# Optimization experiments

Measured on AMD Instinct MI355X. Metric: run time of the kernel, lower is better.

The kernel has to match this reference:

```python
import jax, jax.numpy as jnp
import numpy as np

B, N, T = 16, 10000, 24
E = 160000
H, O = 32, 16  # hidden_channels, out_channels


def setup_inputs() -> dict:
    key = jax.random.key(0)
    ks = jax.random.split(key, 13)
    x = jax.random.normal(ks[0], (B, N, T), jnp.float32)
    edge_index = jax.random.randint(ks[1], (2, E), 0, N)
    edge_weight = jax.random.uniform(ks[2], (E,), jnp.float32)

    def init(k, shape, fan):
        return (jax.random.normal(k, shape, jnp.float32) / np.sqrt(fan)).astype(jnp.float32)

    # torch.nn.GRU params (gate order: r, z, n)
    w_ih = init(ks[3], (3 * H, 1), 1)
    w_hh = init(ks[4], (3 * H, H), H)
    b_ih = jnp.zeros((3 * H,), jnp.float32)
    b_hh = jnp.zeros((3 * H,), jnp.float32)
    # GCNConv weights (stored [in, out]) and biases
    W1 = init(ks[5], (H, H), H)
    b1 = jnp.zeros((H,), jnp.float32)
    W2 = init(ks[6], (H, O), H)
    b2 = jnp.zeros((O,), jnp.float32)
    # final Linear(out_channels, 1), stored [O, 1]
    Wfc = init(ks[7], (O, 1), O)
    bfc = jnp.zeros((1,), jnp.float32)
    return {"x": x, "edge_index": edge_index, "edge_weight": edge_weight,
            "w_ih": w_ih, "w_hh": w_hh, "b_ih": b_ih, "b_hh": b_hh,
            "W1": W1, "b1": b1, "W2": W2, "b2": b2, "Wfc": Wfc, "bfc": bfc}


def _gru_last(x_seq, w_ih, w_hh, b_ih, b_hh):
    # x_seq: [M, T, 1] -> final hidden state [M, H]
    h_dim = w_hh.shape[1]
    xt = jnp.swapaxes(x_seq, 0, 1)            # [T, M, 1]
    gx = xt @ w_ih.T + b_ih                    # precompute input gates [T, M, 3H]

    def step(h, gxt):
        gh = h @ w_hh.T + b_hh
        xr, xz, xn = jnp.split(gxt, 3, axis=-1)
        hr, hz, hn = jnp.split(gh, 3, axis=-1)
        r = jax.nn.sigmoid(xr + hr)
        z = jax.nn.sigmoid(xz + hz)
        n = jnp.tanh(xn + r * hn)
        return (1.0 - z) * n + z * h, None

    h0 = jnp.zeros((x_seq.shape[0], h_dim), x_seq.dtype)
    hT, _ = jax.lax.scan(step, h0, gx)
    return hT


def _gcn_norm(edge_index, edge_weight, n_nodes):
    # PyG gcn_norm with added self-loops (weight 1) and symmetric D^-1/2 A D^-1/2
    loop = jnp.arange(n_nodes)
    src = jnp.concatenate([edge_index[0], loop])
    tgt = jnp.concatenate([edge_index[1], loop])
    w = jnp.concatenate([edge_weight, jnp.ones((n_nodes,), edge_weight.dtype)])
    deg = jax.ops.segment_sum(w, tgt, num_segments=n_nodes)
    dinv = jnp.where(deg > 0, jax.lax.rsqrt(jnp.where(deg > 0, deg, 1.0)), 0.0)
    norm = dinv[src] * w * dinv[tgt]
    return src, tgt, norm


def _gcn_conv(h, W, b, src, tgt, norm):
    # h: [B, N, Fin] -> [B, N, Fout]; gather from src, scatter-add to tgt
    xw = h @ W                                 # [B, N, Fout]
    msg = xw[:, src, :] * norm[None, :, None]  # [B, E+N, Fout]
    out = jnp.zeros_like(xw).at[:, tgt, :].add(msg)
    return out + b


def reference(x, edge_index, edge_weight, w_ih, w_hh, b_ih, b_hh, W1, b1, W2, b2, Wfc, bfc):
    batch, n_nodes, t_len = x.shape
    # GRU temporal encoder per station (eval mode: dropout is identity)
    x_flat = x.reshape(batch * n_nodes, t_len, 1)
    h = _gru_last(x_flat, w_ih, w_hh, b_ih, b_hh).reshape(batch, n_nodes, -1)
    src, tgt, norm = _gcn_norm(edge_index, edge_weight, n_nodes)
    h = jax.nn.relu(_gcn_conv(h, W1, b1, src, tgt, norm))
    h = _gcn_conv(h, W2, b2, src, tgt, norm)
    out = (h @ Wfc + bfc)[..., 0]              # [B, N]
    return out
```

## Files before the change

### kernel.cpp

```cpp
#include <hip/hip_runtime.h>

#define TLEN 24
#define HID 32
#define NNODES 10000

typedef __attribute__((ext_vector_type(8))) short short8;
typedef __attribute__((ext_vector_type(4))) float floatx4;
typedef __attribute__((ext_vector_type(4))) int int4v;

__device__ __forceinline__ unsigned short bf16_rne(float f) {
    unsigned u = __float_as_uint(f);
    unsigned r = u + 0x7fffu + ((u >> 16) & 1u);
    return (unsigned short)(r >> 16);
}
__device__ __forceinline__ float bf16_tof(unsigned short b) {
    return __uint_as_float(((unsigned)b) << 16);
}
__device__ __forceinline__ unsigned cvt_pk_bf16(float a, float b) {
    unsigned r;
    asm("v_cvt_pk_bf16_f32 %0, %1, %2" : "=v"(r) : "v"(a), "v"(b));
    return r;
}
__device__ __forceinline__ void split_pair(float a, float b, unsigned& hi, unsigned& lo) {
    hi = cvt_pk_bf16(a, b);
    float ar = __uint_as_float(hi << 16);
    float br = __uint_as_float(hi & 0xffff0000u);
    lo = cvt_pk_bf16(a - ar, b - br);
}

#define MFMA16(a, b, c) __builtin_amdgcn_mfma_f32_16x16x32_bf16((a), (b), (c), 0, 0, 0)

__global__ __launch_bounds__(256, 3) void gru_xw1_kernel(
    const float* __restrict__ x, const float* __restrict__ w_ih,
    const float* __restrict__ w_hh, const float* __restrict__ b_ih,
    const float* __restrict__ b_hh, const float* __restrict__ W1,
    float* __restrict__ xw1, int BN)
{
    __shared__ float xs[64][25];
    const int tid = threadIdx.x;
    const int wv = tid >> 6, lane = tid & 63;
    const int u = lane >> 4;
    const int s = lane & 15;

    for (int i = tid; i < 64 * TLEN; i += 256) {
        int sl = i / TLEN, t = i - sl * TLEN;
        int gseq = blockIdx.x * 64 + sl;
        if (gseq >= BN) gseq = BN - 1;
        xs[sl][t] = x[(size_t)gseq * TLEN + t];
    }
    __syncthreads();

    const float sc_rz = 1.4426950408889634f;
    const float sc_n  = 2.8853900817779268f;

    const int arow_g = 8 * (s >> 2) + (s & 3);
    short8 wh[6], wl[6];
#pragma unroll
    for (int G = 0; G < 3; G++) {
        float sc = (G == 2) ? sc_n : sc_rz;
#pragma unroll
        for (int hf = 0; hf < 2; hf++) {
            int row = G * 32 + arow_g + 4 * hf;
            const float* wp = w_hh + row * 32 + 8 * u;
            unsigned hib[4], lob[4];
#pragma unroll
            for (int p = 0; p < 4; p++)
                split_pair(wp[2 * p] * sc, wp[2 * p + 1] * sc, hib[p], lob[p]);
            int4v hv = {(int)hib[0], (int)hib[1], (int)hib[2], (int)hib[3]};
            int4v lv = {(int)lob[0], (int)lob[1], (int)lob[2], (int)lob[3]};
            wh[G * 2 + hf] = __builtin_bit_cast(short8, hv);
            wl[G * 2 + hf] = __builtin_bit_cast(short8, lv);
        }
    }

    floatx4 CUR[2], CPR[2], CUZ[2], CPZ[2], CUN[2], CBNI[2], CBNH[2];
#pragma unroll
    for (int hf = 0; hf < 2; hf++) {
#pragma unroll
        for (int r = 0; r < 4; r++) {
            int g = 8 * u + hf * 4 + r;
            CUR[hf][r]  = w_ih[g] * sc_rz;
            CPR[hf][r]  = (b_ih[g] + b_hh[g]) * sc_rz;
            CUZ[hf][r]  = w_ih[32 + g] * sc_rz;
            CPZ[hf][r]  = (b_ih[32 + g] + b_hh[32 + g]) * sc_rz;
            CUN[hf][r]  = w_ih[64 + g] * sc_n;
            CBNI[hf][r] = b_ih[64 + g] * sc_n;
            CBNH[hf][r] = b_hh[64 + g] * sc_n;
        }
    }

    asm volatile("" : "+v"(wh[0]), "+v"(wh[1]), "+v"(wh[2]), "+v"(wh[3]),
                      "+v"(wh[4]), "+v"(wh[5]), "+v"(wl[0]), "+v"(wl[1]),
                      "+v"(wl[2]), "+v"(wl[3]), "+v"(wl[4]), "+v"(wl[5]));
    asm volatile("" : "+v"(CUR[0]), "+v"(CUR[1]), "+v"(CPR[0]), "+v"(CPR[1]),
                      "+v"(CUZ[0]), "+v"(CUZ[1]), "+v"(CPZ[0]), "+v"(CPZ[1]));
    asm volatile("" : "+v"(CUN[0]), "+v"(CUN[1]), "+v"(CBNI[0]), "+v"(CBNI[1]),
                      "+v"(CBNH[0]), "+v"(CBNH[1]));

    float h[8];
#pragma unroll
    for (int i = 0; i < 8; i++) h[i] = 0.f;
    short8 Bh = {0, 0, 0, 0, 0, 0, 0, 0}, Bl = {0, 0, 0, 0, 0, 0, 0, 0};

    const int xrow = wv * 16 + s;

#pragma unroll 1
    for (int t = 0; t < TLEN; t++) {
        float xt = xs[xrow][t];
        floatx4 Dr0, Dr1, Dz0, Dz1;
        floatx4 Dn0 = CBNH[0], Dn1 = CBNH[1];
#pragma unroll
        for (int r = 0; r < 4; r++) {
            Dr0[r] = fmaf(xt, CUR[0][r], CPR[0][r]);
            Dr1[r] = fmaf(xt, CUR[1][r], CPR[1][r]);
            Dz0[r] = fmaf(xt, CUZ[0][r], CPZ[0][r]);
            Dz1[r] = fmaf(xt, CUZ[1][r], CPZ[1][r]);
        }
        Dr0 = MFMA16(wh[0], Bh, Dr0); Dr0 = MFMA16(wh[0], Bl, Dr0); Dr0 = MFMA16(wl[0], Bh, Dr0);
        Dr1 = MFMA16(wh[1], Bh, Dr1); Dr1 = MFMA16(wh[1], Bl, Dr1); Dr1 = MFMA16(wl[1], Bh, Dr1);
        Dz0 = MFMA16(wh[2], Bh, Dz0); Dz0 = MFMA16(wh[2], Bl, Dz0); Dz0 = MFMA16(wl[2], Bh, Dz0);
        Dz1 = MFMA16(wh[3], Bh, Dz1); Dz1 = MFMA16(wh[3], Bl, Dz1); Dz1 = MFMA16(wl[3], Bh, Dz1);
        Dn0 = MFMA16(wh[4], Bh, Dn0); Dn0 = MFMA16(wh[4], Bl, Dn0); Dn0 = MFMA16(wl[4], Bh, Dn0);
        Dn1 = MFMA16(wh[5], Bh, Dn1); Dn1 = MFMA16(wh[5], Bl, Dn1); Dn1 = MFMA16(wl[5], Bh, Dn1);

#pragma unroll
        for (int i = 0; i < 8; i++) {
            float dr = (i < 4) ? Dr0[i] : Dr1[i - 4];
            float dz = (i < 4) ? Dz0[i] : Dz1[i - 4];
            float dn = (i < 4) ? Dn0[i] : Dn1[i - 4];
            float rr = __builtin_amdgcn_rcpf(1.f + __builtin_amdgcn_exp2f(-dr));
            float zz = __builtin_amdgcn_rcpf(1.f + __builtin_amdgcn_exp2f(-dz));
            float gxn = fmaf(xt, CUN[i >> 2][i & 3], CBNI[i >> 2][i & 3]);
            float pn2 = fmaf(rr, dn, gxn);
            float e2 = __builtin_amdgcn_exp2f(pn2);
            float tnh = fmaf(-2.f, __builtin_amdgcn_rcpf(e2 + 1.f), 1.f);
            h[i] = fmaf(zz, h[i] - tnh, tnh);
        }
        unsigned hb[4], lb[4];
#pragma unroll
        for (int p = 0; p < 4; p++) split_pair(h[2 * p], h[2 * p + 1], hb[p], lb[p]);
        int4v hv = {(int)hb[0], (int)hb[1], (int)hb[2], (int)hb[3]};
        int4v lv = {(int)lb[0], (int)lb[1], (int)lb[2], (int)lb[3]};
        Bh = __builtin_bit_cast(short8, hv);
        Bl = __builtin_bit_cast(short8, lv);
    }

    short8 W1h[2], W1l[2];
#pragma unroll
    for (int tile = 0; tile < 2; tile++) {
        int o = tile * 16 + s;
        short8 a, b;
#pragma unroll
        for (int j = 0; j < 8; j++) {
            float wfull = W1[(8 * u + j) * 32 + o];
            unsigned short hbb = bf16_rne(wfull);
            float lo = wfull - bf16_tof(hbb);
            a[j] = (short)hbb;
            b[j] = (short)bf16_rne(lo);
        }
        W1h[tile] = a; W1l[tile] = b;
    }
    floatx4 X0, X1;
#pragma unroll
    for (int r = 0; r < 4; r++) { X0[r] = 0.f; X1[r] = 0.f; }
    X0 = MFMA16(W1h[0], Bh, X0); X0 = MFMA16(W1h[0], Bl, X0); X0 = MFMA16(W1l[0], Bh, X0);
    X1 = MFMA16(W1h[1], Bh, X1); X1 = MFMA16(W1h[1], Bl, X1); X1 = MFMA16(W1l[1], Bh, X1);

    int seq = blockIdx.x * 64 + wv * 16 + s;
    if (seq >= BN) seq = BN - 1;
    int bq = seq / NNODES;
    int nn = seq - bq * NNODES;
    float* base = xw1 + (size_t)nn * 512 + bq * 32 + 4 * u;
    float4 v0, v1;
    v0.x = X0[0]; v0.y = X0[1]; v0.z = X0[2]; v0.w = X0[3];
    v1.x = X1[0]; v1.y = X1[1]; v1.z = X1[2]; v1.w = X1[3];
    *reinterpret_cast<float4*>(base) = v0;
    *reinterpret_cast<float4*>(base + 16) = v1;
}

__global__ void init_deg_cnt(float* deg, int* cnt, int N)
{
    int i = blockIdx.x * 256 + threadIdx.x;
    if (i < N) { deg[i] = 1.0f; cnt[i] = 1; }
}

__global__ void deg_accum(const int* __restrict__ src, const int* __restrict__ tgt,
                          const float* __restrict__ ew, float* deg, int* cnt, int E)
{
    int e = blockIdx.x * 256 + threadIdx.x;
    if (e < E) {
        int t = tgt[e];
        atomicAdd(&deg[t], ew[e]);
        atomicAdd(&cnt[t], 1);
    }
}

__global__ void dinv_kernel(const float* __restrict__ deg, float* dinv, int N)
{
    int i = blockIdx.x * 256 + threadIdx.x;
    if (i < N) {
        float d = deg[i];
        dinv[i] = d > 0.f ? rsqrtf(d) : 0.f;
    }
}

__global__ __launch_bounds__(1024) void scan_kernel(
    const int* __restrict__ cnt, int* offs, int* cursor, int N)
{
    __shared__ int part[1024];
    const int tid = threadIdx.x;
    const int CH = (N + 1023) / 1024;
    const int base = tid * CH;
    int sum = 0;
    for (int k = 0; k < CH; k++) {
        int i = base + k;
        if (i < N) sum += cnt[i];
    }
    part[tid] = sum;
    __syncthreads();
    for (int ofs = 1; ofs < 1024; ofs <<= 1) {
        int v = (tid >= ofs) ? part[tid - ofs] : 0;
        __syncthreads();
        part[tid] += v;
        __syncthreads();
    }
    int run = part[tid] - sum;
    if (tid == 0) offs[0] = 0;
    for (int k = 0; k < CH; k++) {
        int i = base + k;
        if (i < N) {
            int c = cnt[i];
            cursor[i] = run;
            run += c;
            offs[i + 1] = run;
        }
    }
}

__global__ void fill_csr(const int* __restrict__ src, const int* __restrict__ tgt,
                         const float* __restrict__ ew, const float* __restrict__ dinv,
                         int* cursor, int* csr_src, float* csr_norm, int E, int N)
{
    int i = blockIdx.x * 256 + threadIdx.x;
    if (i < E) {
        int s = src[i], t = tgt[i];
        int pos = atomicAdd(&cursor[t], 1);
        csr_src[pos] = s;
        csr_norm[pos] = dinv[s] * ew[i] * dinv[t];
    } else if (i < E + N) {
        int n = i - E;
        int pos = atomicAdd(&cursor[n], 1);
        csr_src[pos] = n;
        csr_norm[pos] = dinv[n] * dinv[n];
    }
}

__global__ __launch_bounds__(256) void conv1y_kernel(
    const float* __restrict__ xw1, const int* __restrict__ offs,
    const int* __restrict__ csrc, const float* __restrict__ cnorm,
    const float* __restrict__ b1, const float* __restrict__ W2,
    const float* __restrict__ Wfc, float* __restrict__ y, int N)
{
    int n = __builtin_amdgcn_readfirstlane((blockIdx.x << 2) + (threadIdx.x >> 6));
    if (n >= N) return;
    int lane = threadIdx.x & 63;
    int b = lane >> 2, f4 = lane & 3;

    float vf[8], bf[8];
#pragma unroll
    for (int j = 0; j < 8; j++) {
        int f = f4 * 8 + j;
        float a = 0.f;
#pragma unroll
        for (int o = 0; o < 16; o++) a = fmaf(W2[f * 16 + o], Wfc[o], a);
        vf[j] = a;
        bf[j] = b1[f];
    }

    int beg = __builtin_amdgcn_readfirstlane(offs[n]);
    int end = __builtin_amdgcn_readfirstlane(offs[n + 1]);
    float acc[8];
#pragma unroll
    for (int j = 0; j < 8; j++) acc[j] = 0.f;

    for (int i = beg; i < end; i++) {
        int s = csrc[i];
        float wn = cnorm[i];
        const float4* p = reinterpret_cast<const float4*>(xw1 + (size_t)s * 512 + lane * 8);
        float4 v0 = p[0], v1 = p[1];
        acc[0] = fmaf(wn, v0.x, acc[0]);
        acc[1] = fmaf(wn, v0.y, acc[1]);
        acc[2] = fmaf(wn, v0.z, acc[2]);
        acc[3] = fmaf(wn, v0.w, acc[3]);
        acc[4] = fmaf(wn, v1.x, acc[4]);
        acc[5] = fmaf(wn, v1.y, acc[5]);
        acc[6] = fmaf(wn, v1.z, acc[6]);
        acc[7] = fmaf(wn, v1.w, acc[7]);
    }

    float val = 0.f;
#pragma unroll
    for (int j = 0; j < 8; j++)
        val = fmaf(fmaxf(acc[j] + bf[j], 0.f), vf[j], val);
    val += __shfl_xor(val, 1);
    val += __shfl_xor(val, 2);
    if (f4 == 0) y[n * 16 + b] = val;
}

__global__ __launch_bounds__(256) void conv2out_kernel(
    const float* __restrict__ y, const int* __restrict__ offs,
    const int* __restrict__ csrc, const float* __restrict__ cnorm,
    const float* __restrict__ b2, const float* __restrict__ Wfc,
    const float* __restrict__ bfc, float* __restrict__ out, int N)
{
    int n = __builtin_amdgcn_readfirstlane((blockIdx.x << 2) + (threadIdx.x >> 6));
    if (n >= N) return;
    int lane = threadIdx.x & 63;
    int b = lane & 15, e = lane >> 4;
    float c = bfc[0];
#pragma unroll
    for (int o = 0; o < 16; o++) c = fmaf(b2[o], Wfc[o], c);
    int beg = __builtin_amdgcn_readfirstlane(offs[n]);
    int end = __builtin_amdgcn_readfirstlane(offs[n + 1]);
    float acc = 0.f;
    for (int i = beg + e; i < end; i += 4) {
        int s = csrc[i];
        acc = fmaf(cnorm[i], y[s * 16 + b], acc);
    }
    acc += __shfl_xor(acc, 16);
    acc += __shfl_xor(acc, 32);
    if (lane < 16) out[b * N + n] = acc + c;
}

extern "C" void kernel_launch(void* const* d_in, const int* in_sizes, int n_in,
                              void* d_out, int out_size, void* d_ws, size_t ws_size,
                              hipStream_t stream)
{
    const float* x    = (const float*)d_in[0];
    const int*   eidx = (const int*)d_in[1];
    const float* ew   = (const float*)d_in[2];
    const float* w_ih = (const float*)d_in[3];
    const float* w_hh = (const float*)d_in[4];
    const float* b_ih = (const float*)d_in[5];
    const float* b_hh = (const float*)d_in[6];
    const float* W1   = (const float*)d_in[7];
    const float* b1   = (const float*)d_in[8];
    const float* W2   = (const float*)d_in[9];
    const float* b2   = (const float*)d_in[10];
    const float* Wfc  = (const float*)d_in[11];
    const float* bfc  = (const float*)d_in[12];

    const int E  = in_sizes[2];
    const int BN = in_sizes[0] / TLEN;
    const int N  = NNODES;
    const int* esrc = eidx;
    const int* etgt = eidx + E;
    float* out = (float*)d_out;

    char* w = (char*)d_ws;
    auto alloc = [&](size_t bytes) -> char* {
        char* p = w;
        w += (bytes + 255) / 256 * 256;
        return p;
    };
    float* xw1      = (float*)alloc((size_t)BN * 32 * 4);
    float* y        = (float*)alloc((size_t)N * 16 * 4);
    float* deg      = (float*)alloc((size_t)N * 4);
    float* dinv     = (float*)alloc((size_t)N * 4);
    int*   cnt      = (int*)alloc((size_t)N * 4);
    int*   offs     = (int*)alloc((size_t)(N + 4) * 4);
    int*   cursor   = (int*)alloc((size_t)N * 4);
    int*   csr_src  = (int*)alloc((size_t)(E + N) * 4);
    float* csr_norm = (float*)alloc((size_t)(E + N) * 4);

    hipLaunchKernelGGL(init_deg_cnt, dim3((N + 255) / 256), dim3(256), 0, stream, deg, cnt, N);
    hipLaunchKernelGGL(deg_accum, dim3((E + 255) / 256), dim3(256), 0, stream, esrc, etgt, ew, deg, cnt, E);
    hipLaunchKernelGGL(dinv_kernel, dim3((N + 255) / 256), dim3(256), 0, stream, deg, dinv, N);
    hipLaunchKernelGGL(scan_kernel, dim3(1), dim3(1024), 0, stream, cnt, offs, cursor, N);
    hipLaunchKernelGGL(fill_csr, dim3((E + N + 255) / 256), dim3(256), 0, stream,
                       esrc, etgt, ew, dinv, cursor, csr_src, csr_norm, E, N);

    hipLaunchKernelGGL(gru_xw1_kernel, dim3((BN + 63) / 64), dim3(256), 0, stream,
                       x, w_ih, w_hh, b_ih, b_hh, W1, xw1, BN);
    hipLaunchKernelGGL(conv1y_kernel, dim3((N + 3) / 4), dim3(256), 0, stream,
                       xw1, offs, csr_src, csr_norm, b1, W2, Wfc, y, N);
    hipLaunchKernelGGL(conv2out_kernel, dim3((N + 3) / 4), dim3(256), 0, stream,
                       y, offs, csr_src, csr_norm, b2, Wfc, bfc, out, N);
}
```

Measured before the change: 247.8 us.

## Store xw1 intermediate in fp16, prefetch gather rows, fuse dinv into scan

Stores the GRU+W1 output xw1 as fp16 instead of fp32, halving the bytes written by the GRU kernel and gathered per edge in the first GCN aggregation. The aggregation loop now loads the next neighbour row and weight one iteration ahead so the gather latency overlaps the FMAs. The separate dinv kernel is merged into the single-block scan kernel to save a launch. The cost is reduced precision in the intermediate features and more serial work inside the one-block scan.

```diff
diff --git a/kernel.cpp b/kernel.cpp
--- a/kernel.cpp
+++ b/kernel.cpp
@@ -7,6 +7,8 @@
 typedef __attribute__((ext_vector_type(8))) short short8;
 typedef __attribute__((ext_vector_type(4))) float floatx4;
 typedef __attribute__((ext_vector_type(4))) int int4v;
+typedef __attribute__((ext_vector_type(4))) _Float16 half4;
+typedef __attribute__((ext_vector_type(8))) _Float16 half8;
 
 __device__ __forceinline__ unsigned short bf16_rne(float f) {
     unsigned u = __float_as_uint(f);
@@ -34,7 +36,7 @@
     const float* __restrict__ x, const float* __restrict__ w_ih,
     const float* __restrict__ w_hh, const float* __restrict__ b_ih,
     const float* __restrict__ b_hh, const float* __restrict__ W1,
-    float* __restrict__ xw1, int BN)
+    _Float16* __restrict__ xw1, int BN)
 {
     __shared__ float xs[64][25];
     const int tid = threadIdx.x;
@@ -170,12 +172,12 @@
     if (seq >= BN) seq = BN - 1;
     int bq = seq / NNODES;
     int nn = seq - bq * NNODES;
-    float* base = xw1 + (size_t)nn * 512 + bq * 32 + 4 * u;
-    float4 v0, v1;
-    v0.x = X0[0]; v0.y = X0[1]; v0.z = X0[2]; v0.w = X0[3];
-    v1.x = X1[0]; v1.y = X1[1]; v1.z = X1[2]; v1.w = X1[3];
-    *reinterpret_cast<float4*>(base) = v0;
-    *reinterpret_cast<float4*>(base + 16) = v1;
+    _Float16* base = xw1 + (size_t)nn * 512 + bq * 32 + 4 * u;
+    half4 o0, o1;
+#pragma unroll
+    for (int r = 0; r < 4; r++) { o0[r] = (_Float16)X0[r]; o1[r] = (_Float16)X1[r]; }
+    *reinterpret_cast<half4*>(base) = o0;
+    *reinterpret_cast<half4*>(base + 16) = o1;
 }
 
 __global__ void init_deg_cnt(float* deg, int* cnt, int N)
@@ -195,17 +197,9 @@
     }
 }
 
-__global__ void dinv_kernel(const float* __restrict__ deg, float* dinv, int N)
-{
-    int i = blockIdx.x * 256 + threadIdx.x;
-    if (i < N) {
-        float d = deg[i];
-        dinv[i] = d > 0.f ? rsqrtf(d) : 0.f;
-    }
-}
-
 __global__ __launch_bounds__(1024) void scan_kernel(
-    const int* __restrict__ cnt, int* offs, int* cursor, int N)
+    const int* __restrict__ cnt, const float* __restrict__ deg,
+    float* __restrict__ dinv, int* offs, int* cursor, int N)
 {
     __shared__ int part[1024];
     const int tid = threadIdx.x;
@@ -214,7 +208,11 @@
     int sum = 0;
     for (int k = 0; k < CH; k++) {
         int i = base + k;
-        if (i < N) sum += cnt[i];
+        if (i < N) {
+            sum += cnt[i];
+            float d = deg[i];
+            dinv[i] = d > 0.f ? __frsqrt_rn(d) : 0.f;
+        }
     }
     part[tid] = sum;
     __syncthreads();
@@ -256,7 +254,7 @@
 }
 
 __global__ __launch_bounds__(256) void conv1y_kernel(
-    const float* __restrict__ xw1, const int* __restrict__ offs,
+    const _Float16* __restrict__ xw1, const int* __restrict__ offs,
     const int* __restrict__ csrc, const float* __restrict__ cnorm,
     const float* __restrict__ b1, const float* __restrict__ W2,
     const float* __restrict__ Wfc, float* __restrict__ y, int N)
@@ -283,19 +281,19 @@
 #pragma unroll
     for (int j = 0; j < 8; j++) acc[j] = 0.f;
 
+    float wcur = cnorm[beg];
+    half8 vcur = *reinterpret_cast<const half8*>(xw1 + (size_t)csrc[beg] * 512 + lane * 8);
     for (int i = beg; i < end; i++) {
-        int s = csrc[i];
-        float wn = cnorm[i];
-        const float4* p = reinterpret_cast<const float4*>(xw1 + (size_t)s * 512 + lane * 8);
-        float4 v0 = p[0], v1 = p[1];
-        acc[0] = fmaf(wn, v0.x, acc[0]);
-        acc[1] = fmaf(wn, v0.y, acc[1]);
-        acc[2] = fmaf(wn, v0.z, acc[2]);
-        acc[3] = fmaf(wn, v0.w, acc[3]);
-        acc[4] = fmaf(wn, v1.x, acc[4]);
-        acc[5] = fmaf(wn, v1.y, acc[5]);
-        acc[6] = fmaf(wn, v1.z, acc[6]);
-        acc[7] = fmaf(wn, v1.w, acc[7]);
+        float wnext = 0.f;
+        half8 vnext = vcur;
+        if (i + 1 < end) {
+            wnext = cnorm[i + 1];
+            vnext = *reinterpret_cast<const half8*>(xw1 + (size_t)csrc[i + 1] * 512 + lane * 8);
+        }
+#pragma unroll
+        for (int j = 0; j < 8; j++) acc[j] = fmaf(wcur, (float)vcur[j], acc[j]);
+        wcur = wnext;
+        vcur = vnext;
     }
 
     float val = 0.f;
@@ -363,7 +361,7 @@
         w += (bytes + 255) / 256 * 256;
         return p;
     };
-    float* xw1      = (float*)alloc((size_t)BN * 32 * 4);
+    _Float16* xw1   = (_Float16*)alloc((size_t)BN * 32 * 2);
     float* y        = (float*)alloc((size_t)N * 16 * 4);
     float* deg      = (float*)alloc((size_t)N * 4);
     float* dinv     = (float*)alloc((size_t)N * 4);
@@ -375,8 +373,7 @@
 
     hipLaunchKernelGGL(init_deg_cnt, dim3((N + 255) / 256), dim3(256), 0, stream, deg, cnt, N);
     hipLaunchKernelGGL(deg_accum, dim3((E + 255) / 256), dim3(256), 0, stream, esrc, etgt, ew, deg, cnt, E);
-    hipLaunchKernelGGL(dinv_kernel, dim3((N + 255) / 256), dim3(256), 0, stream, deg, dinv, N);
-    hipLaunchKernelGGL(scan_kernel, dim3(1), dim3(1024), 0, stream, cnt, offs, cursor, N);
+    hipLaunchKernelGGL(scan_kernel, dim3(1), dim3(1024), 0, stream, cnt, deg, dinv, offs, cursor, N);
     hipLaunchKernelGGL(fill_csr, dim3((E + N + 255) / 256), dim3(256), 0, stream,
                        esrc, etgt, ew, dinv, cursor, csr_src, csr_norm, E, N);
 
```

Measured after the change: 244.4 us. No clear change (-1.4%).
